# Performance work log

Hardware: AMD Instinct MI355X
Metric: run time of the kernel (lower is better)

Reference implementation:

```python
import jax, jax.numpy as jnp
import numpy as np

B, N, C = 2, 3072, 768
H = 12                      # num_heads
HD = C // H                 # 64
D = HD // 2                 # 32, rope dim per axis
GRID_H, GRID_W = 48, 64     # 768/16, 1024/16 ; GRID_H*GRID_W == N
BASE = 100.0
EPS = 1e-5


def _rope_tables():
    # positions per token (row-major cartesian product of y,x)
    pos_y = np.repeat(np.arange(GRID_H), GRID_W)   # [N]
    pos_x = np.tile(np.arange(GRID_W), GRID_H)     # [N]
    seq_len = max(GRID_H, GRID_W)
    inv_freq = 1.0 / BASE ** (np.arange(0, D, 2, dtype=np.float32) / D)  # [D/2]
    t = np.arange(seq_len, dtype=np.float32)
    freqs = np.einsum('i,j->ij', t, inv_freq)            # [S, D/2]
    emb = np.concatenate([freqs, freqs], axis=-1)        # [S, D]
    cos, sin = np.cos(emb), np.sin(emb)
    # gather per-token, add head broadcast dims -> [1, 1, N, D]
    mk = lambda tbl, idx: jnp.asarray(tbl[idx][None, None], dtype=jnp.float32)
    return mk(cos, pos_x), mk(sin, pos_x), mk(cos, pos_y), mk(sin, pos_y)


def setup_inputs() -> dict:
    key = jax.random.key(0)
    ks = jax.random.split(key, 12)
    s = 0.02
    cos_x, sin_x, cos_y, sin_y = _rope_tables()
    return {
        'x': jax.random.normal(ks[0], (B, N, C), jnp.float32),
        'w_qkv': jax.random.normal(ks[1], (3 * C, C), jnp.float32) * s,
        'w_proj': jax.random.normal(ks[2], (C, C), jnp.float32) * s,
        'b_proj': jnp.zeros((C,), jnp.float32),
        'g1': jnp.ones((C,), jnp.float32),
        'beta1': jnp.zeros((C,), jnp.float32),
        'g2': jnp.ones((C,), jnp.float32),
        'beta2': jnp.zeros((C,), jnp.float32),
        'w_fc1': jax.random.normal(ks[3], (4 * C, C), jnp.float32) * s,
        'b_fc1': jnp.zeros((4 * C,), jnp.float32),
        'w_fc2': jax.random.normal(ks[4], (C, 4 * C), jnp.float32) * s,
        'b_fc2': jnp.zeros((C,), jnp.float32),
        'cos_x': cos_x, 'sin_x': sin_x, 'cos_y': cos_y, 'sin_y': sin_y,
    }


def _layernorm(x, g, b):
    m = x.mean(-1, keepdims=True)
    v = ((x - m) ** 2).mean(-1, keepdims=True)
    return (x - m) * jax.lax.rsqrt(v + EPS) * g + b


def _rope1d(tok, cos, sin):
    t1, t2 = jnp.split(tok, 2, axis=-1)
    rot = jnp.concatenate([-t2, t1], axis=-1)
    return tok * cos + rot * sin


def _rope2d(tok, cos_x, sin_x, cos_y, sin_y):
    # tok: [B, H, N, HD]; first half of HD is y-coords, second half x-coords
    ty, tx = jnp.split(tok, 2, axis=-1)
    return jnp.concatenate([_rope1d(ty, cos_y, sin_y), _rope1d(tx, cos_x, sin_x)], axis=-1)


def reference(x, w_qkv, w_proj, b_proj, g1, beta1, g2, beta2,
              w_fc1, b_fc1, w_fc2, b_fc2, cos_x, sin_x, cos_y, sin_y):
    # --- attention branch ---
    xn = _layernorm(x, g1, beta1)
    qkv = jnp.einsum('bnc,dc->bnd', xn, w_qkv)           # [B, N, 3C]
    qkv = qkv.reshape(B, N, 3, H, HD).transpose(0, 3, 2, 1, 4)  # [B, H, 3, N, HD]
    q, k, v = qkv[:, :, 0], qkv[:, :, 1], qkv[:, :, 2]
    q = _rope2d(q, cos_x, sin_x, cos_y, sin_y)
    k = _rope2d(k, cos_x, sin_x, cos_y, sin_y)
    scale = HD ** -0.5
    attn = jnp.einsum('bhqd,bhkd->bhqk', q, k) * scale   # [B, H, N, N]
    attn = jax.nn.softmax(attn, axis=-1)
    o = jnp.einsum('bhqk,bhkd->bhqd', attn, v)           # [B, H, N, HD]
    o = o.transpose(0, 2, 1, 3).reshape(B, N, C)
    o = jnp.einsum('bnc,dc->bnd', o, w_proj) + b_proj
    x = x + o
    # --- mlp branch ---
    xn = _layernorm(x, g2, beta2)
    h = jnp.einsum('bnc,hc->bnh', xn, w_fc1) + b_fc1
    h = jax.nn.gelu(h, approximate=False)                # torch nn.GELU default (erf)
    h = jnp.einsum('bnh,ch->bnc', h, w_fc2) + b_fc2
    return x + h
```

## Files before the change

### kernel.cpp

```cpp
#include <hip/hip_runtime.h>
#include <hip/hip_bf16.h>


#define Nn 3072
#define Cc 768
#define Hh 12
#define Mm 6144

typedef unsigned short ushort_t;
typedef unsigned int u32;
using s8v = __attribute__((ext_vector_type(8))) short;
using f4v = __attribute__((ext_vector_type(4))) float;

__device__ __forceinline__ ushort_t f2b(float x){
  u32 u = __float_as_uint(x);
  return (ushort_t)((u + 0x7fffu + ((u >> 16) & 1u)) >> 16);
}
__device__ __forceinline__ u32 pack2(float a, float b){
  return (u32)f2b(a) | ((u32)f2b(b) << 16);
}
__device__ __forceinline__ u32 pack2t(float a, float b){
  return (__float_as_uint(a) >> 16) | (__float_as_uint(b) & 0xffff0000u);
}
__device__ __forceinline__ float b2f(ushort_t u){
  return __uint_as_float(((u32)u) << 16);
}

#define GLD16(g, l) __builtin_amdgcn_global_load_lds( \
    (const __attribute__((address_space(1))) u32*)(g), \
    (__attribute__((address_space(3))) u32*)(l), 16, 0, 0)

__global__ __launch_bounds__(256) void cvt4_kernel(
    const float* __restrict__ a, ushort_t* __restrict__ oa, int na,
    const float* __restrict__ b, ushort_t* __restrict__ ob, int nb,
    const float* __restrict__ c, ushort_t* __restrict__ oc, int nc,
    const float* __restrict__ d, ushort_t* __restrict__ od)
{
  int i = (blockIdx.x*256 + threadIdx.x)*4;
  const float* src; ushort_t* dst;
  if (i < na)           { src = a + i;            dst = oa + i; }
  else if (i < na+nb)   { src = b + (i-na);       dst = ob + (i-na); }
  else if (i < na+nb+nc){ src = c + (i-na-nb);    dst = oc + (i-na-nb); }
  else                  { src = d + (i-na-nb-nc); dst = od + (i-na-nb-nc); }
  float4 v = *(const float4*)src;
  uint2 p; p.x = pack2(v.x, v.y); p.y = pack2(v.z, v.w);
  *(uint2*)dst = p;
}

__global__ __launch_bounds__(256) void ln_kernel(const float* __restrict__ in,
    const float* __restrict__ g, const float* __restrict__ be, ushort_t* __restrict__ out)
{
  int row = blockIdx.x;
  int tid = threadIdx.x;
  size_t base = (size_t)row * Cc;
  float v[3];
  #pragma unroll
  for (int i = 0; i < 3; ++i) v[i] = in[base + tid + i*256];
  __shared__ float red[8];
  float s = v[0]+v[1]+v[2];
  #pragma unroll
  for (int off=32; off; off>>=1) s += __shfl_xor(s, off);
  int wid = tid >> 6, lane = tid & 63;
  if (lane==0) red[wid] = s;
  __syncthreads();
  float mean = (red[0]+red[1]+red[2]+red[3]) * (1.f/Cc);
  float d = 0.f;
  #pragma unroll
  for (int i=0;i<3;++i){ float t = v[i]-mean; d += t*t; }
  #pragma unroll
  for (int off=32; off; off>>=1) d += __shfl_xor(d, off);
  if (lane==0) red[4+wid] = d;
  __syncthreads();
  float var  = (red[4]+red[5]+red[6]+red[7]) * (1.f/Cc);
  float rstd = rsqrtf(var + 1e-5f);
  #pragma unroll
  for (int i=0;i<3;++i){
    int idx = tid + i*256;
    out[base+idx] = f2b((v[i]-mean)*rstd*g[idx] + be[idx]);
  }
}

template<int EPI, int NT>
__global__ __launch_bounds__(256) void mgemm_kernel(
    const ushort_t* __restrict__ A, const ushort_t* __restrict__ W,
    const float* __restrict__ bias, const float* __restrict__ residf,
    void* __restrict__ outv, int Nd, int K)
{
  constexpr int JT = NT/32;
  __shared__ __align__(16) ushort_t As[2][128*32];
  __shared__ __align__(16) ushort_t Ws[2][NT*32];
  int tid = threadIdx.x;
  int w = tid >> 6, lane = tid & 63;
  int g = lane >> 4, c = lane & 15;
  int wr = w >> 1, wc = w & 1;
  int gx = gridDim.x;
  int nwg = gx * gridDim.y;
  int lin = blockIdx.y * gx + blockIdx.x;
  int swz = (lin & 7) * (nwg >> 3) + (lin >> 3);
  int bx = swz % gx, by = swz / gx;
  int m0 = by * 128, n0 = bx * NT;
  int schunk = (lane & 3) * 8;
  const ushort_t* Ag = A + (size_t)(m0 + w*32 + (lane >> 2))*K + schunk;
  const ushort_t* Wg;
  if constexpr (NT == 128) Wg = W + (size_t)(n0 + w*32 + (lane >> 2))*K + schunk;
  else                     Wg = W + (size_t)(n0 + w*16 + (lane >> 2))*K + schunk;
  int wAoff = w*1024;
  int wWoff = (NT == 128) ? w*1024 : w*512;
  f4v acc[4][JT] = {};

  {
    GLD16(Ag,        &As[0][wAoff]);
    GLD16(Ag + 16*K, &As[0][wAoff + 512]);
    GLD16(Wg,        &Ws[0][wWoff]);
    if constexpr (NT == 128) GLD16(Wg + 16*K, &Ws[0][wWoff + 512]);
  }
  __syncthreads();

  int nk = K >> 5;
  for (int t = 0; t < nk; ++t) {
    int cur = t & 1;
    if (t + 1 < nk) {
      int k1 = (t + 1) << 5;
      GLD16(Ag + k1,        &As[cur^1][wAoff]);
      GLD16(Ag + 16*K + k1, &As[cur^1][wAoff + 512]);
      GLD16(Wg + k1,        &Ws[cur^1][wWoff]);
      if constexpr (NT == 128) GLD16(Wg + 16*K + k1, &Ws[cur^1][wWoff + 512]);
    }
    s8v af[4], wf[JT];
    #pragma unroll
    for (int i=0;i<4;++i) af[i] = *(const s8v*)&As[cur][(wr*64 + i*16 + c)*32 + g*8];
    #pragma unroll
    for (int j=0;j<JT;++j) wf[j] = *(const s8v*)&Ws[cur][(wc*(NT/2) + j*16 + c)*32 + g*8];
    #pragma unroll
    for (int i=0;i<4;++i)
      #pragma unroll
      for (int j=0;j<JT;++j)
        acc[i][j] = __builtin_amdgcn_mfma_f32_16x16x32_bf16(af[i], wf[j], acc[i][j], 0,0,0);
    __syncthreads();
  }
  #pragma unroll
  for (int j=0;j<JT;++j){
    int col = n0 + wc*(NT/2) + j*16 + c;
    float bv = (EPI != 0) ? bias[col] : 0.f;
    #pragma unroll
    for (int i=0;i<4;++i){
      int row0 = m0 + wr*64 + i*16 + g*4;
      #pragma unroll
      for (int r=0;r<4;++r){
        float v = acc[i][j][r];
        size_t off = (size_t)(row0 + r)*Nd + col;
        if (EPI == 0) {
          ((ushort_t*)outv)[off] = f2b(v);
        } else if (EPI == 2) {
          float t = v + bv;
          ((ushort_t*)outv)[off] = f2b(0.5f*t*(1.0f + erff(t*0.70710678118654752f)));
        } else {
          ((float*)outv)[off] = v + bv + residf[off];
        }
      }
    }
  }
}

__global__ __launch_bounds__(256) void repack_kernel(
    const ushort_t* __restrict__ qkv,
    const float* __restrict__ cx, const float* __restrict__ sx,
    const float* __restrict__ cy, const float* __restrict__ sy,
    ushort_t* __restrict__ Qb, ushort_t* __restrict__ Kb, ushort_t* __restrict__ Vt)
{
  __shared__ float Vls[64*68];
  int bh = blockIdx.y;
  int b = bh / Hh, h = bh - b*Hh;
  int n0 = blockIdx.x * 64;
  int tid = threadIdx.x;
  int tt = tid >> 2, cch = tid & 3;
  int n = n0 + tt;
  size_t rowbase = (size_t)(b*Nn + n) * 2304 + h*64;

  int half = cch >> 1, ibase = (cch & 1) * 8;
  int d1 = half*32 + ibase;
  const float* ct  = half ? cx : cy;
  const float* st_ = half ? sx : sy;
  float c1[8], s1[8], c2[8], s2[8];
  #pragma unroll
  for (int j=0;j<8;++j){
    c1[j] = ct[n*32 + ibase + j];       s1[j] = st_[n*32 + ibase + j];
    c2[j] = ct[n*32 + ibase + 16 + j];  s2[j] = st_[n*32 + ibase + 16 + j];
  }
  #pragma unroll
  for (int qk = 0; qk < 2; ++qk){
    const ushort_t* src = qkv + rowbase + qk*768;
    uint4 uv1 = *(const uint4*)(src + d1);
    uint4 uv2 = *(const uint4*)(src + d1 + 16);
    float v1[8], v2[8];
    v1[0]=b2f(uv1.x&0xffff); v1[1]=b2f(uv1.x>>16); v1[2]=b2f(uv1.y&0xffff); v1[3]=b2f(uv1.y>>16);
    v1[4]=b2f(uv1.z&0xffff); v1[5]=b2f(uv1.z>>16); v1[6]=b2f(uv1.w&0xffff); v1[7]=b2f(uv1.w>>16);
    v2[0]=b2f(uv2.x&0xffff); v2[1]=b2f(uv2.x>>16); v2[2]=b2f(uv2.y&0xffff); v2[3]=b2f(uv2.y>>16);
    v2[4]=b2f(uv2.z&0xffff); v2[5]=b2f(uv2.z>>16); v2[6]=b2f(uv2.w&0xffff); v2[7]=b2f(uv2.w>>16);
    float sc = qk ? 1.0f : 0.18033688011112042f;
    float o1[8], o2[8];
    #pragma unroll
    for (int j=0;j<8;++j){
      o1[j] = (v1[j]*c1[j] - v2[j]*s1[j]) * sc;
      o2[j] = (v2[j]*c2[j] + v1[j]*s2[j]) * sc;
    }
    ushort_t* dst = (qk ? Kb : Qb) + ((size_t)bh*Nn + n)*64;
    uint4 u1, u2;
    u1.x = pack2(o1[0],o1[1]); u1.y = pack2(o1[2],o1[3]);
    u1.z = pack2(o1[4],o1[5]); u1.w = pack2(o1[6],o1[7]);
    u2.x = pack2(o2[0],o2[1]); u2.y = pack2(o2[2],o2[3]);
    u2.z = pack2(o2[4],o2[5]); u2.w = pack2(o2[6],o2[7]);
    *(uint4*)(dst + d1)      = u1;
    *(uint4*)(dst + d1 + 16) = u2;
  }

  {
    const ushort_t* src = qkv + rowbase + 1536 + cch*16;
    uint4 ua = *(const uint4*)(src);
    uint4 ub = *(const uint4*)(src + 8);
    float* lp = &Vls[tt*68 + cch*16];
    lp[0]=b2f(ua.x&0xffff); lp[1]=b2f(ua.x>>16); lp[2]=b2f(ua.y&0xffff); lp[3]=b2f(ua.y>>16);
    lp[4]=b2f(ua.z&0xffff); lp[5]=b2f(ua.z>>16); lp[6]=b2f(ua.w&0xffff); lp[7]=b2f(ua.w>>16);
    lp[8]=b2f(ub.x&0xffff); lp[9]=b2f(ub.x>>16); lp[10]=b2f(ub.y&0xffff); lp[11]=b2f(ub.y>>16);
    lp[12]=b2f(ub.z&0xffff); lp[13]=b2f(ub.z>>16); lp[14]=b2f(ub.w&0xffff); lp[15]=b2f(ub.w>>16);
  }
  __syncthreads();
  {
    int d = tid & 63, quarter = tid >> 6;
    float v[16];
    #pragma unroll
    for (int j=0;j<16;++j) v[j] = Vls[(quarter*16 + j)*68 + d];
    uint4 w0, w1;
    w0.x = pack2(v[0],v[1]);   w0.y = pack2(v[2],v[3]);
    w0.z = pack2(v[4],v[5]);   w0.w = pack2(v[6],v[7]);
    w1.x = pack2(v[8],v[9]);   w1.y = pack2(v[10],v[11]);
    w1.z = pack2(v[12],v[13]); w1.w = pack2(v[14],v[15]);
    ushort_t* dst = Vt + ((size_t)bh*64 + d)*Nn + n0 + quarter*16;
    *(uint4*)(dst)     = w0;
    *(uint4*)(dst + 8) = w1;
  }
}

__global__ __launch_bounds__(256, 3) void fattn_kernel(
    const ushort_t* __restrict__ Qb, const ushort_t* __restrict__ Kb,
    const ushort_t* __restrict__ Vt, ushort_t* __restrict__ ob)
{
  __shared__ __align__(16) char smem[36864];
  __shared__ float Lred[256];
  int bh = blockIdx.x;
  int q0 = blockIdx.y * 64;
  int tid = threadIdx.x;
  int w = tid >> 6, lane = tid & 63, g = lane >> 4, c = lane & 15;

  const ushort_t* kbase = Kb + (size_t)bh*Nn*64;
  const ushort_t* vbase = Vt + (size_t)bh*64*Nn;

  s8v qf0[4], qf1[4];
  #pragma unroll
  for (int qs=0;qs<4;++qs){
    const ushort_t* qp = Qb + ((size_t)bh*Nn + q0 + qs*16 + c)*64;
    qf0[qs] = *(const s8v*)(qp + g*8);
    qf1[qs] = *(const s8v*)(qp + 32 + g*8);
  }
  s8v ones8;
  #pragma unroll
  for (int j=0;j<8;++j) ones8[j] = (short)0x3f80;

  f4v o[4][4] = {};
  f4v l[4] = {};
  ushort_t* pw = (ushort_t*)smem + w*4608;

  for (int it = 0; it < 12; ++it){
    int key0 = (it*4 + w) * 64;
    s8v ka[4], kb2[4];
    #pragma unroll
    for (int ks=0;ks<4;++ks){
      const ushort_t* kr = kbase + (size_t)(key0 + ks*16 + c)*64 + g*8;
      ka[ks]  = *(const s8v*)(kr);
      kb2[ks] = *(const s8v*)(kr + 32);
    }
    #pragma unroll
    for (int qs=0;qs<4;++qs){
      #pragma unroll
      for (int ks=0;ks<4;++ks){
        f4v z = {0,0,0,0};
        z = __builtin_amdgcn_mfma_f32_16x16x32_bf16(ka[ks],  qf0[qs], z, 0,0,0);
        z = __builtin_amdgcn_mfma_f32_16x16x32_bf16(kb2[ks], qf1[qs], z, 0,0,0);
        uint2 pk;
        pk.x = pack2t(__builtin_amdgcn_exp2f(z[0]), __builtin_amdgcn_exp2f(z[1]));
        pk.y = pack2t(__builtin_amdgcn_exp2f(z[2]), __builtin_amdgcn_exp2f(z[3]));
        *(uint2*)&pw[qs*1152 + c*72 + ks*16 + g*4] = pk;
      }
    }
    asm volatile("s_waitcnt lgkmcnt(0)" ::: "memory");
    s8v va[4], vb[4];
    #pragma unroll
    for (int d=0;d<4;++d){
      const ushort_t* vr = vbase + (size_t)(d*16 + c)*Nn + key0 + g*8;
      va[d] = *(const s8v*)(vr);
      vb[d] = *(const s8v*)(vr + 32);
    }
    #pragma unroll
    for (int qs=0;qs<4;++qs){
      s8v pf0 = *(const s8v*)&pw[qs*1152 + c*72 + g*8];
      s8v pf1 = *(const s8v*)&pw[qs*1152 + c*72 + 32 + g*8];
      #pragma unroll
      for (int d=0;d<4;++d){
        o[qs][d] = __builtin_amdgcn_mfma_f32_16x16x32_bf16(va[d], pf0, o[qs][d], 0,0,0);
        o[qs][d] = __builtin_amdgcn_mfma_f32_16x16x32_bf16(vb[d], pf1, o[qs][d], 0,0,0);
      }
      l[qs] = __builtin_amdgcn_mfma_f32_16x16x32_bf16(ones8, pf0, l[qs], 0,0,0);
      l[qs] = __builtin_amdgcn_mfma_f32_16x16x32_bf16(ones8, pf1, l[qs], 0,0,0);
    }
  }

  ushort_t* Or = (ushort_t*)smem;
  #pragma unroll
  for (int qs=0;qs<4;++qs){
    #pragma unroll
    for (int d=0;d<4;++d){
      uint2 pk;
      pk.x = pack2(o[qs][d][0], o[qs][d][1]);
      pk.y = pack2(o[qs][d][2], o[qs][d][3]);
      *(uint2*)&Or[(w*64 + qs*16 + c)*72 + d*16 + g*4] = pk;
    }
    Lred[w*64 + qs*16 + c] = l[qs][0];
  }
  __syncthreads();

  int qrow = tid >> 2, dseg = (tid & 3) * 16;
  float acc[16] = {};
  #pragma unroll
  for (int w2=0;w2<4;++w2){
    const ushort_t* base = &Or[(w2*64 + qrow)*72 + dseg];
    uint4 u0 = *(const uint4*)(base);
    uint4 u1 = *(const uint4*)(base + 8);
    u32 uu[8] = {u0.x,u0.y,u0.z,u0.w,u1.x,u1.y,u1.z,u1.w};
    #pragma unroll
    for (int j=0;j<8;++j){
      acc[j*2]   += b2f((ushort_t)(uu[j] & 0xffff));
      acc[j*2+1] += b2f((ushort_t)(uu[j] >> 16));
    }
  }
  float rl = 1.0f / (Lred[qrow] + Lred[64+qrow] + Lred[128+qrow] + Lred[192+qrow]);
  int b = bh / Hh, h = bh - b*Hh;
  ushort_t* op = ob + ((size_t)b*Nn + q0 + qrow)*768 + h*64 + dseg;
  uint4 w0_, w1_;
  w0_.x = pack2(acc[0]*rl, acc[1]*rl);   w0_.y = pack2(acc[2]*rl, acc[3]*rl);
  w0_.z = pack2(acc[4]*rl, acc[5]*rl);   w0_.w = pack2(acc[6]*rl, acc[7]*rl);
  w1_.x = pack2(acc[8]*rl, acc[9]*rl);   w1_.y = pack2(acc[10]*rl, acc[11]*rl);
  w1_.z = pack2(acc[12]*rl, acc[13]*rl); w1_.w = pack2(acc[14]*rl, acc[15]*rl);
  *(uint4*)(op)     = w0_;
  *(uint4*)(op + 8) = w1_;
}

extern "C" void kernel_launch(void* const* d_in, const int* in_sizes, int n_in,
                              void* d_out, int out_size, void* d_ws, size_t ws_size,
                              hipStream_t stream)
{
  const float* x      = (const float*)d_in[0];
  const float* w_qkv  = (const float*)d_in[1];
  const float* w_proj = (const float*)d_in[2];
  const float* b_proj = (const float*)d_in[3];
  const float* g1     = (const float*)d_in[4];
  const float* be1    = (const float*)d_in[5];
  const float* g2     = (const float*)d_in[6];
  const float* be2    = (const float*)d_in[7];
  const float* w_fc1  = (const float*)d_in[8];
  const float* b_fc1  = (const float*)d_in[9];
  const float* w_fc2  = (const float*)d_in[10];
  const float* b_fc2  = (const float*)d_in[11];
  const float* cx     = (const float*)d_in[12];
  const float* sx     = (const float*)d_in[13];
  const float* cy     = (const float*)d_in[14];
  const float* sy     = (const float*)d_in[15];
  float* out = (float*)d_out;

  char* ws = (char*)d_ws;
  ushort_t* xnb   = (ushort_t*)(ws);
  ushort_t* Qb    = (ushort_t*)(ws + 9437184);
  ushort_t* Kb    = (ushort_t*)(ws + 18874368);
  float*    x1    = (float*)   (ws + 9437184);
  ushort_t* Vt    = (ushort_t*)(ws + 28311552);
  ushort_t* obb   = (ushort_t*)(ws + 37748736);
  ushort_t* qkvb  = (ushort_t*)(ws + 47185920);
  ushort_t* hb    = (ushort_t*)(ws + 47185920);
  ushort_t* wqkvb = (ushort_t*)(ws + 84934656);
  ushort_t* wprojb= (ushort_t*)(ws + 88473600);
  ushort_t* wfc1b = (ushort_t*)(ws + 89653248);
  ushort_t* wfc2b = (ushort_t*)(ws + 94371840);

  cvt4_kernel<<<(7077888/4)/256, 256, 0, stream>>>(
      w_qkv, wqkvb, 2304*768, w_proj, wprojb, 768*768,
      w_fc1, wfc1b, 3072*768, w_fc2, wfc2b);

  ln_kernel<<<Mm, 256, 0, stream>>>(x, g1, be1, xnb);
  mgemm_kernel<0,128><<<dim3(2304/128, Mm/128), 256, 0, stream>>>(xnb, wqkvb, nullptr, nullptr, qkvb, 2304, 768);
  repack_kernel<<<dim3(48, 24), 256, 0, stream>>>(qkvb, cx, sx, cy, sy, Qb, Kb, Vt);
  fattn_kernel<<<dim3(24, 48), 256, 0, stream>>>(Qb, Kb, Vt, obb);
  mgemm_kernel<1,64><<<dim3(768/64, Mm/128), 256, 0, stream>>>(obb, wprojb, b_proj, x, x1, 768, 768);
  ln_kernel<<<Mm, 256, 0, stream>>>(x1, g2, be2, xnb);
  mgemm_kernel<2,128><<<dim3(3072/128, Mm/128), 256, 0, stream>>>(xnb, wfc1b, b_fc1, nullptr, hb, 3072, 768);
  mgemm_kernel<1,64><<<dim3(768/64, Mm/128), 256, 0, stream>>>(hb, wfc2b, b_fc2, x1, out, 768, 3072);
}
```

Baseline: 438.4 us.

## Fuse RoPE and V-transpose into QKV GEMM epilogue; merge weight cast with LN1

Replaces the QKV GEMM + repack pair with a single GEMM kernel whose epilogue applies 2D RoPE and Q scaling and writes Q/K per head, and writes V transposed directly. This removes the bf16 qkv intermediate round-trip and one launch. The weight conversion and first layernorm are merged into one launch via block-index dispatch. The epilogue stores are scalar 2-byte writes for Q/K and strided 8-byte writes for V, which may be less coalesced than the old repack.

Measured after the change: 422.8 us. -3.6%, faster.

```diff
diff --git a/kernel.cpp b/kernel.cpp
--- a/kernel.cpp
+++ b/kernel.cpp
@@ -6,6 +6,7 @@
 #define Cc 768
 #define Hh 12
 #define Mm 6144
+#define CVTBLKS 6912
 
 typedef unsigned short ushort_t;
 typedef unsigned int u32;
@@ -30,21 +31,54 @@
     (const __attribute__((address_space(1))) u32*)(g), \
     (__attribute__((address_space(3))) u32*)(l), 16, 0, 0)
 
-__global__ __launch_bounds__(256) void cvt4_kernel(
+__global__ __launch_bounds__(256) void cvtln_kernel(
     const float* __restrict__ a, ushort_t* __restrict__ oa, int na,
     const float* __restrict__ b, ushort_t* __restrict__ ob, int nb,
     const float* __restrict__ c, ushort_t* __restrict__ oc, int nc,
-    const float* __restrict__ d, ushort_t* __restrict__ od)
-{
-  int i = (blockIdx.x*256 + threadIdx.x)*4;
-  const float* src; ushort_t* dst;
-  if (i < na)           { src = a + i;            dst = oa + i; }
-  else if (i < na+nb)   { src = b + (i-na);       dst = ob + (i-na); }
-  else if (i < na+nb+nc){ src = c + (i-na-nb);    dst = oc + (i-na-nb); }
-  else                  { src = d + (i-na-nb-nc); dst = od + (i-na-nb-nc); }
-  float4 v = *(const float4*)src;
-  uint2 p; p.x = pack2(v.x, v.y); p.y = pack2(v.z, v.w);
-  *(uint2*)dst = p;
+    const float* __restrict__ d, ushort_t* __restrict__ od,
+    const float* __restrict__ xin, const float* __restrict__ g1,
+    const float* __restrict__ be1, ushort_t* __restrict__ xout)
+{
+  int tid = threadIdx.x;
+  if (blockIdx.x < CVTBLKS) {
+    int i = (blockIdx.x*256 + tid)*4;
+    const float* src; ushort_t* dst;
+    if (i < na)           { src = a + i;            dst = oa + i; }
+    else if (i < na+nb)   { src = b + (i-na);       dst = ob + (i-na); }
+    else if (i < na+nb+nc){ src = c + (i-na-nb);    dst = oc + (i-na-nb); }
+    else                  { src = d + (i-na-nb-nc); dst = od + (i-na-nb-nc); }
+    float4 v = *(const float4*)src;
+    uint2 p; p.x = pack2(v.x, v.y); p.y = pack2(v.z, v.w);
+    *(uint2*)dst = p;
+    return;
+  }
+  int row = blockIdx.x - CVTBLKS;
+  size_t base = (size_t)row * Cc;
+  float v[3];
+  #pragma unroll
+  for (int i = 0; i < 3; ++i) v[i] = xin[base + tid + i*256];
+  __shared__ float red[8];
+  float s = v[0]+v[1]+v[2];
+  #pragma unroll
+  for (int off=32; off; off>>=1) s += __shfl_xor(s, off);
+  int wid = tid >> 6, lane = tid & 63;
+  if (lane==0) red[wid] = s;
+  __syncthreads();
+  float mean = (red[0]+red[1]+red[2]+red[3]) * (1.f/Cc);
+  float dd = 0.f;
+  #pragma unroll
+  for (int i=0;i<3;++i){ float t = v[i]-mean; dd += t*t; }
+  #pragma unroll
+  for (int off=32; off; off>>=1) dd += __shfl_xor(dd, off);
+  if (lane==0) red[4+wid] = dd;
+  __syncthreads();
+  float var  = (red[4]+red[5]+red[6]+red[7]) * (1.f/Cc);
+  float rstd = rsqrtf(var + 1e-5f);
+  #pragma unroll
+  for (int i=0;i<3;++i){
+    int idx = tid + i*256;
+    xout[base+idx] = f2b((v[i]-mean)*rstd*g1[idx] + be1[idx]);
+  }
 }
 
 __global__ __launch_bounds__(256) void ln_kernel(const float* __restrict__ in,
@@ -141,7 +175,7 @@
   #pragma unroll
   for (int j=0;j<JT;++j){
     int col = n0 + wc*(NT/2) + j*16 + c;
-    float bv = (EPI != 0) ? bias[col] : 0.f;
+    float bv = bias[col];
     #pragma unroll
     for (int i=0;i<4;++i){
       int row0 = m0 + wr*64 + i*16 + g*4;
@@ -149,9 +183,7 @@
       for (int r=0;r<4;++r){
         float v = acc[i][j][r];
         size_t off = (size_t)(row0 + r)*Nd + col;
-        if (EPI == 0) {
-          ((ushort_t*)outv)[off] = f2b(v);
-        } else if (EPI == 2) {
+        if (EPI == 2) {
           float t = v + bv;
           ((ushort_t*)outv)[off] = f2b(0.5f*t*(1.0f + erff(t*0.70710678118654752f)));
         } else {
@@ -162,82 +194,104 @@
   }
 }
 
-__global__ __launch_bounds__(256) void repack_kernel(
-    const ushort_t* __restrict__ qkv,
+__global__ __launch_bounds__(256) void qkvgemm_kernel(
+    const ushort_t* __restrict__ A, const ushort_t* __restrict__ W,
     const float* __restrict__ cx, const float* __restrict__ sx,
     const float* __restrict__ cy, const float* __restrict__ sy,
     ushort_t* __restrict__ Qb, ushort_t* __restrict__ Kb, ushort_t* __restrict__ Vt)
 {
-  __shared__ float Vls[64*68];
-  int bh = blockIdx.y;
-  int b = bh / Hh, h = bh - b*Hh;
-  int n0 = blockIdx.x * 64;
+  constexpr int NT = 128, JT = 4, K = 768;
+  __shared__ __align__(16) ushort_t As[2][128*32];
+  __shared__ __align__(16) ushort_t Ws[2][NT*32];
   int tid = threadIdx.x;
-  int tt = tid >> 2, cch = tid & 3;
-  int n = n0 + tt;
-  size_t rowbase = (size_t)(b*Nn + n) * 2304 + h*64;
-
-  int half = cch >> 1, ibase = (cch & 1) * 8;
-  int d1 = half*32 + ibase;
-  const float* ct  = half ? cx : cy;
-  const float* st_ = half ? sx : sy;
-  float c1[8], s1[8], c2[8], s2[8];
-  #pragma unroll
-  for (int j=0;j<8;++j){
-    c1[j] = ct[n*32 + ibase + j];       s1[j] = st_[n*32 + ibase + j];
-    c2[j] = ct[n*32 + ibase + 16 + j];  s2[j] = st_[n*32 + ibase + 16 + j];
-  }
-  #pragma unroll
-  for (int qk = 0; qk < 2; ++qk){
-    const ushort_t* src = qkv + rowbase + qk*768;
-    uint4 uv1 = *(const uint4*)(src + d1);
-    uint4 uv2 = *(const uint4*)(src + d1 + 16);
-    float v1[8], v2[8];
-    v1[0]=b2f(uv1.x&0xffff); v1[1]=b2f(uv1.x>>16); v1[2]=b2f(uv1.y&0xffff); v1[3]=b2f(uv1.y>>16);
-    v1[4]=b2f(uv1.z&0xffff); v1[5]=b2f(uv1.z>>16); v1[6]=b2f(uv1.w&0xffff); v1[7]=b2f(uv1.w>>16);
-    v2[0]=b2f(uv2.x&0xffff); v2[1]=b2f(uv2.x>>16); v2[2]=b2f(uv2.y&0xffff); v2[3]=b2f(uv2.y>>16);
-    v2[4]=b2f(uv2.z&0xffff); v2[5]=b2f(uv2.z>>16); v2[6]=b2f(uv2.w&0xffff); v2[7]=b2f(uv2.w>>16);
-    float sc = qk ? 1.0f : 0.18033688011112042f;
-    float o1[8], o2[8];
-    #pragma unroll
-    for (int j=0;j<8;++j){
-      o1[j] = (v1[j]*c1[j] - v2[j]*s1[j]) * sc;
-      o2[j] = (v2[j]*c2[j] + v1[j]*s2[j]) * sc;
-    }
-    ushort_t* dst = (qk ? Kb : Qb) + ((size_t)bh*Nn + n)*64;
-    uint4 u1, u2;
-    u1.x = pack2(o1[0],o1[1]); u1.y = pack2(o1[2],o1[3]);
-    u1.z = pack2(o1[4],o1[5]); u1.w = pack2(o1[6],o1[7]);
-    u2.x = pack2(o2[0],o2[1]); u2.y = pack2(o2[2],o2[3]);
-    u2.z = pack2(o2[4],o2[5]); u2.w = pack2(o2[6],o2[7]);
-    *(uint4*)(dst + d1)      = u1;
-    *(uint4*)(dst + d1 + 16) = u2;
-  }
+  int w = tid >> 6, lane = tid & 63;
+  int g = lane >> 4, c = lane & 15;
+  int wr = w >> 1, wc = w & 1;
+  int gx = gridDim.x;
+  int nwg = gx * gridDim.y;
+  int lin = blockIdx.y * gx + blockIdx.x;
+  int swz = (lin & 7) * (nwg >> 3) + (lin >> 3);
+  int bx = swz % gx, by = swz / gx;
+  int m0 = by * 128, n0 = bx * NT;
+  int schunk = (lane & 3) * 8;
+  const ushort_t* Ag = A + (size_t)(m0 + w*32 + (lane >> 2))*K + schunk;
+  const ushort_t* Wg = W + (size_t)(n0 + w*32 + (lane >> 2))*K + schunk;
+  int wAoff = w*1024;
+  f4v acc[4][JT] = {};
 
   {
-    const ushort_t* src = qkv + rowbase + 1536 + cch*16;
-    uint4 ua = *(const uint4*)(src);
-    uint4 ub = *(const uint4*)(src + 8);
-    float* lp = &Vls[tt*68 + cch*16];
-    lp[0]=b2f(ua.x&0xffff); lp[1]=b2f(ua.x>>16); lp[2]=b2f(ua.y&0xffff); lp[3]=b2f(ua.y>>16);
-    lp[4]=b2f(ua.z&0xffff); lp[5]=b2f(ua.z>>16); lp[6]=b2f(ua.w&0xffff); lp[7]=b2f(ua.w>>16);
-    lp[8]=b2f(ub.x&0xffff); lp[9]=b2f(ub.x>>16); lp[10]=b2f(ub.y&0xffff); lp[11]=b2f(ub.y>>16);
-    lp[12]=b2f(ub.z&0xffff); lp[13]=b2f(ub.z>>16); lp[14]=b2f(ub.w&0xffff); lp[15]=b2f(ub.w>>16);
-  }
-  __syncthreads();
-  {
-    int d = tid & 63, quarter = tid >> 6;
-    float v[16];
-    #pragma unroll
-    for (int j=0;j<16;++j) v[j] = Vls[(quarter*16 + j)*68 + d];
-    uint4 w0, w1;
-    w0.x = pack2(v[0],v[1]);   w0.y = pack2(v[2],v[3]);
-    w0.z = pack2(v[4],v[5]);   w0.w = pack2(v[6],v[7]);
-    w1.x = pack2(v[8],v[9]);   w1.y = pack2(v[10],v[11]);
-    w1.z = pack2(v[12],v[13]); w1.w = pack2(v[14],v[15]);
-    ushort_t* dst = Vt + ((size_t)bh*64 + d)*Nn + n0 + quarter*16;
-    *(uint4*)(dst)     = w0;
-    *(uint4*)(dst + 8) = w1;
+    GLD16(Ag,        &As[0][wAoff]);
+    GLD16(Ag + 16*K, &As[0][wAoff + 512]);
+    GLD16(Wg,        &Ws[0][wAoff]);
+    GLD16(Wg + 16*K, &Ws[0][wAoff + 512]);
+  }
+  __syncthreads();
+
+  int nk = K >> 5;
+  for (int t = 0; t < nk; ++t) {
+    int cur = t & 1;
+    if (t + 1 < nk) {
+      int k1 = (t + 1) << 5;
+      GLD16(Ag + k1,        &As[cur^1][wAoff]);
+      GLD16(Ag + 16*K + k1, &As[cur^1][wAoff + 512]);
+      GLD16(Wg + k1,        &Ws[cur^1][wAoff]);
+      GLD16(Wg + 16*K + k1, &Ws[cur^1][wAoff + 512]);
+    }
+    s8v af[4], wf[JT];
+    #pragma unroll
+    for (int i=0;i<4;++i) af[i] = *(const s8v*)&As[cur][(wr*64 + i*16 + c)*32 + g*8];
+    #pragma unroll
+    for (int j=0;j<JT;++j) wf[j] = *(const s8v*)&Ws[cur][(wc*64 + j*16 + c)*32 + g*8];
+    #pragma unroll
+    for (int i=0;i<4;++i)
+      #pragma unroll
+      for (int j=0;j<JT;++j)
+        acc[i][j] = __builtin_amdgcn_mfma_f32_16x16x32_bf16(af[i], wf[j], acc[i][j], 0,0,0);
+    __syncthreads();
+  }
+
+  int region = n0 / 768;
+  int h = ((n0 - region*768) >> 6) + wc;
+  if (region < 2) {
+    float sc = region ? 1.0f : 0.18033688011112042f;
+    ushort_t* dstb = region ? Kb : Qb;
+    #pragma unroll
+    for (int i=0;i<4;++i){
+      int row0 = m0 + wr*64 + i*16 + g*4;
+      #pragma unroll
+      for (int r=0;r<4;++r){
+        int row = row0 + r;
+        int b = row >= Nn;
+        int nt = row - (b ? Nn : 0);
+        size_t tb = (size_t)nt*32 + c;
+        float vlo0 = acc[i][0][r], vhi0 = acc[i][1][r];
+        float vlo1 = acc[i][2][r], vhi1 = acc[i][3][r];
+        float o0 = (vlo0*cy[tb]    - vhi0*sy[tb])    * sc;
+        float o1 = (vhi0*cy[tb+16] + vlo0*sy[tb+16]) * sc;
+        float o2 = (vlo1*cx[tb]    - vhi1*sx[tb])    * sc;
+        float o3 = (vhi1*cx[tb+16] + vlo1*sx[tb+16]) * sc;
+        ushort_t* dp = dstb + ((size_t)(b*Hh + h)*Nn + nt)*64;
+        dp[c]      = f2b(o0);
+        dp[16 + c] = f2b(o1);
+        dp[32 + c] = f2b(o2);
+        dp[48 + c] = f2b(o3);
+      }
+    }
+  } else {
+    #pragma unroll
+    for (int i=0;i<4;++i){
+      int row0 = m0 + wr*64 + i*16 + g*4;
+      int b = row0 >= Nn;
+      int nt0 = row0 - (b ? Nn : 0);
+      #pragma unroll
+      for (int j=0;j<4;++j){
+        int d = j*16 + c;
+        uint2 pk;
+        pk.x = pack2(acc[i][j][0], acc[i][j][1]);
+        pk.y = pack2(acc[i][j][2], acc[i][j][3]);
+        *(uint2*)&Vt[((size_t)(b*Hh + h)*64 + d)*Nn + nt0] = pk;
+      }
+    }
   }
 }
 
@@ -383,20 +437,19 @@
   float*    x1    = (float*)   (ws + 9437184);
   ushort_t* Vt    = (ushort_t*)(ws + 28311552);
   ushort_t* obb   = (ushort_t*)(ws + 37748736);
-  ushort_t* qkvb  = (ushort_t*)(ws + 47185920);
   ushort_t* hb    = (ushort_t*)(ws + 47185920);
   ushort_t* wqkvb = (ushort_t*)(ws + 84934656);
   ushort_t* wprojb= (ushort_t*)(ws + 88473600);
   ushort_t* wfc1b = (ushort_t*)(ws + 89653248);
   ushort_t* wfc2b = (ushort_t*)(ws + 94371840);
 
-  cvt4_kernel<<<(7077888/4)/256, 256, 0, stream>>>(
+  cvtln_kernel<<<CVTBLKS + Mm, 256, 0, stream>>>(
       w_qkv, wqkvb, 2304*768, w_proj, wprojb, 768*768,
-      w_fc1, wfc1b, 3072*768, w_fc2, wfc2b);
-
-  ln_kernel<<<Mm, 256, 0, stream>>>(x, g1, be1, xnb);
-  mgemm_kernel<0,128><<<dim3(2304/128, Mm/128), 256, 0, stream>>>(xnb, wqkvb, nullptr, nullptr, qkvb, 2304, 768);
-  repack_kernel<<<dim3(48, 24), 256, 0, stream>>>(qkvb, cx, sx, cy, sy, Qb, Kb, Vt);
+      w_fc1, wfc1b, 3072*768, w_fc2, wfc2b,
+      x, g1, be1, xnb);
+
+  qkvgemm_kernel<<<dim3(2304/128, Mm/128), 256, 0, stream>>>(
+      xnb, wqkvb, cx, sx, cy, sy, Qb, Kb, Vt);
   fattn_kernel<<<dim3(24, 48), 256, 0, stream>>>(Qb, Kb, Vt, obb);
   mgemm_kernel<1,64><<<dim3(768/64, Mm/128), 256, 0, stream>>>(obb, wprojb, b_proj, x, x1, 768, 768);
   ln_kernel<<<Mm, 256, 0, stream>>>(x1, g2, be2, xnb);
```
